# Optimization experiments

Measured on AMD Instinct MI355X. Metric: run time of the kernel, lower is better.

## Reference

```python
import jax, jax.numpy as jnp
import numpy as np

EPS = 1e-5

def conv1x1(h, w, b):
    # h: [B,C,H,W], w: [O,C], b: [O]
    return jnp.einsum('bchw,oc->bohw', h, w) + b[None, :, None, None]

def setup_inputs() -> dict:
    key = jax.random.key(0)
    ks = jax.random.split(key, 10)
    B, C, H, W = 4, 256, 64, 64
    x = jax.random.normal(ks[0], (B, C, H, W), dtype=jnp.float32)
    s = 0.02
    return {
        'x': x,
        'gamma': jnp.ones((C,), jnp.float32),
        'beta': jnp.zeros((C,), jnp.float32),
        'wq': jax.random.normal(ks[1], (C, C), jnp.float32) * s,
        'bq': jnp.zeros((C,), jnp.float32),
        'wk': jax.random.normal(ks[2], (C, C), jnp.float32) * s,
        'bk': jnp.zeros((C,), jnp.float32),
        'wv': jax.random.normal(ks[3], (C, C), jnp.float32) * s,
        'bv': jnp.zeros((C,), jnp.float32),
        'wp': jax.random.normal(ks[4], (C, C), jnp.float32) * s,
        'bp': jnp.zeros((C,), jnp.float32),
    }

def reference(x, gamma, beta, wq, bq, wk, bk, wv, bv, wp, bp):
    B, C, H, W = x.shape
    N = H * W
    # BatchNorm2d (training mode: batch statistics, biased variance)
    mean = jnp.mean(x, axis=(0, 2, 3))
    var = jnp.var(x, axis=(0, 2, 3))
    h = (x - mean[None, :, None, None]) * jax.lax.rsqrt(var + EPS)[None, :, None, None]
    h = h * gamma[None, :, None, None] + beta[None, :, None, None]
    q = conv1x1(h, wq, bq).reshape(B, C, N)
    k = conv1x1(h, wk, bk).reshape(B, C, N)
    v = conv1x1(h, wv, bv).reshape(B, C, N)
    # scores[b,i,j] = q_i . k_j, softmax over j (keys)
    scores = jnp.einsum('bci,bcj->bij', q, k) * (C ** -0.5)
    attn = jax.nn.softmax(scores, axis=2)
    # out[b,c,i] = sum_j attn[b,i,j] * v[b,c,j]
    out = jnp.einsum('bij,bcj->bci', attn, v).reshape(B, C, H, W)
    out = conv1x1(out, wp, bp)
    return x + out
```

## Files before the change

kernel.cpp:

```cpp
#include <hip/hip_runtime.h>
#include <cstdint>
#include <cstddef>

#define B_ 4
#define C_ 256
#define N_ 4096

typedef __attribute__((ext_vector_type(8))) short s8v;
typedef __attribute__((ext_vector_type(4))) float f4v;

#if defined(__has_builtin)
#if __has_builtin(__builtin_amdgcn_exp2f)
#define EXP2(x) __builtin_amdgcn_exp2f(x)
#endif
#endif
#ifndef EXP2
#define EXP2(x) exp2f(x)
#endif

__device__ __forceinline__ unsigned short f2bf(float f) {
  unsigned int u = __builtin_bit_cast(unsigned int, f);
  return (unsigned short)((u + 0x7FFFu + ((u >> 16) & 1u)) >> 16);
}

__device__ __forceinline__ unsigned pk2bf_trunc(float lo, float hi) {
  return __builtin_amdgcn_perm(__builtin_bit_cast(unsigned, hi),
                               __builtin_bit_cast(unsigned, lo), 0x07060302u);
}


__global__ __launch_bounds__(256) void bn_stats(const float* __restrict__ x,
                                                float* __restrict__ mean,
                                                float* __restrict__ rstd) {
  int c = blockIdx.x, t = threadIdx.x;
  float s = 0.f, s2 = 0.f;
  for (int b = 0; b < B_; ++b) {
    const float* p = x + ((size_t)b * C_ + c) * N_;
    for (int n = t; n < N_; n += 256) { float v = p[n]; s += v; s2 += v * v; }
  }
  __shared__ float rs[256], rs2[256];
  rs[t] = s; rs2[t] = s2; __syncthreads();
  for (int off = 128; off > 0; off >>= 1) {
    if (t < off) { rs[t] += rs[t + off]; rs2[t] += rs2[t + off]; }
    __syncthreads();
  }
  if (t == 0) {
    float m = rs[0] * (1.f / 16384.f);
    float v = rs2[0] * (1.f / 16384.f) - m * m;
    mean[c] = m; rstd[c] = rsqrtf(v + 1e-5f);
  }
}

__global__ __launch_bounds__(256) void prep(
    const float* __restrict__ wq, const float* __restrict__ bq,
    const float* __restrict__ wk, const float* __restrict__ bk,
    const float* __restrict__ wv, const float* __restrict__ bv,
    const float* __restrict__ wp,
    const float* __restrict__ gamma, const float* __restrict__ beta,
    const float* __restrict__ mean, const float* __restrict__ rstd,
    unsigned short* __restrict__ wqb, unsigned short* __restrict__ wkb,
    unsigned short* __restrict__ wvb, unsigned short* __restrict__ wpb,
    float* __restrict__ beq, float* __restrict__ bek, float* __restrict__ bev) {
  const float QSC = 0.0625f * 1.4426950408889634f;
  int o = blockIdx.x, c = threadIdx.x;
  float a = gamma[c] * rstd[c];
  float d = beta[c] - mean[c] * a;
  float wqv = wq[o * C_ + c], wkv = wk[o * C_ + c], wvv = wv[o * C_ + c];
  wqb[o * C_ + c] = f2bf(wqv * a * QSC);
  wkb[o * C_ + c] = f2bf(wkv * a);
  wvb[o * C_ + c] = f2bf(wvv * a);
  wpb[o * C_ + c] = f2bf(wp[o * C_ + c]);
  __shared__ float r0[256], r1[256], r2[256];
  r0[c] = wqv * d; r1[c] = wkv * d; r2[c] = wvv * d; __syncthreads();
  for (int off = 128; off > 0; off >>= 1) {
    if (c < off) { r0[c] += r0[c + off]; r1[c] += r1[c + off]; r2[c] += r2[c + off]; }
    __syncthreads();
  }
  if (c == 0) {
    beq[o] = (bq[o] + r0[0]) * QSC;
    bek[o] = bk[o] + r1[0];
    bev[o] = bv[o] + r2[0];
  }
}

__global__ __launch_bounds__(256) void xt(const float* __restrict__ x,
                                          unsigned short* __restrict__ xbB) {
  int b = blockIdx.z, c0 = blockIdx.y * 64, n0 = blockIdx.x * 64;
  int tid = threadIdx.x;
  __shared__ unsigned short Ls[64][72];
  int cw = tid >> 6, nl = tid & 63;
#pragma unroll
  for (int rr = 0; rr < 16; ++rr) {
    int c = c0 + cw * 16 + rr;
    Ls[nl][cw * 16 + rr] = f2bf(x[((size_t)b * C_ + c) * N_ + n0 + nl]);
  }
  __syncthreads();
  int n_ = tid >> 2, cs = (tid & 3) * 16;
  s8v v0 = *(const s8v*)(&Ls[n_][cs]);
  s8v v1 = *(const s8v*)(&Ls[n_][cs + 8]);
  int n = n0 + n_;
  size_t base = (((size_t)b * 256 + (n >> 4)) * 32 + ((c0 + cs) >> 3)) * 128 + (n & 15) * 8;
  *(s8v*)(xbB + base) = v0;
  *(s8v*)(xbB + base + 128) = v1;
}

__global__ __launch_bounds__(256) void qkv(
    const unsigned short* __restrict__ xbB,
    const unsigned short* __restrict__ wqb, const unsigned short* __restrict__ wkb,
    const unsigned short* __restrict__ wvb,
    const float* __restrict__ beq, const float* __restrict__ bek,
    const float* __restrict__ bev,
    unsigned short* __restrict__ qB, unsigned short* __restrict__ kB,
    unsigned short* __restrict__ vB) {
  int b = blockIdx.z, oblk = blockIdx.y, n0 = blockIdx.x * 64;
  int tid = threadIdx.x, w = tid >> 6, l = tid & 63, quad = l >> 4, lq = l & 15;
  int orow = oblk * 64 + w * 16 + lq;

  f4v aq[4], ak[4], av[4];
#pragma unroll
  for (int nt = 0; nt < 4; ++nt) {
    aq[nt] = (f4v){0.f, 0.f, 0.f, 0.f};
    ak[nt] = (f4v){0.f, 0.f, 0.f, 0.f};
    av[nt] = (f4v){0.f, 0.f, 0.f, 0.f};
  }

#pragma unroll
  for (int kk = 0; kk < 8; ++kk) {
    s8v afq = *(const s8v*)(wqb + (size_t)orow * C_ + kk * 32 + quad * 8);
    s8v afk = *(const s8v*)(wkb + (size_t)orow * C_ + kk * 32 + quad * 8);
    s8v afv = *(const s8v*)(wvb + (size_t)orow * C_ + kk * 32 + quad * 8);
#pragma unroll
    for (int nt = 0; nt < 4; ++nt) {
      s8v bf = *(const s8v*)(xbB + (((size_t)b * 256 + ((n0 + nt * 16) >> 4)) * 32 + kk * 4 + quad) * 128 + lq * 8);
      aq[nt] = __builtin_amdgcn_mfma_f32_16x16x32_bf16(afq, bf, aq[nt], 0, 0, 0);
      ak[nt] = __builtin_amdgcn_mfma_f32_16x16x32_bf16(afk, bf, ak[nt], 0, 0, 0);
      av[nt] = __builtin_amdgcn_mfma_f32_16x16x32_bf16(afv, bf, av[nt], 0, 0, 0);
    }
  }

  __shared__ unsigned short Ls[64][72];
  int obase = oblk * 64;

  for (int pass = 0; pass < 2; ++pass) {
    const f4v* acc = (pass == 0) ? aq : ak;
    const float* BE = (pass == 0) ? beq : bek;
    unsigned short* dst = (pass == 0) ? qB : kB;
    int ob4 = obase + w * 16 + quad * 4;
    float b0 = BE[ob4], b1 = BE[ob4 + 1], b2 = BE[ob4 + 2], b3 = BE[ob4 + 3];
#pragma unroll
    for (int nt = 0; nt < 4; ++nt) {
      unsigned lo = (unsigned)f2bf(acc[nt][0] + b0) | ((unsigned)f2bf(acc[nt][1] + b1) << 16);
      unsigned hi = (unsigned)f2bf(acc[nt][2] + b2) | ((unsigned)f2bf(acc[nt][3] + b3) << 16);
      uint2 pr; pr.x = lo; pr.y = hi;
      *(uint2*)(&Ls[nt * 16 + lq][w * 16 + quad * 4]) = pr;
    }
    __syncthreads();
    {
      int n16rel = tid >> 6, g_rel = (tid >> 3) & 7, lq2 = (tid & 7) * 2;
      s8v v0 = *(const s8v*)(&Ls[n16rel * 16 + lq2][g_rel * 8]);
      s8v v1 = *(const s8v*)(&Ls[n16rel * 16 + lq2 + 1][g_rel * 8]);
      size_t base = (((size_t)b * 256 + (n0 >> 4) + n16rel) * 32 + (obase >> 3) + g_rel) * 128 + lq2 * 8;
      *(s8v*)(dst + base) = v0;
      *(s8v*)(dst + base + 8) = v1;
    }
    __syncthreads();
  }

#pragma unroll
  for (int nt = 0; nt < 4; ++nt)
#pragma unroll
    for (int r = 0; r < 4; ++r) {
      int o_ = obase + w * 16 + quad * 4 + r;
      Ls[w * 16 + quad * 4 + r][nt * 16 + lq] = f2bf(av[nt][r] + bev[o_]);
    }
  __syncthreads();
  {
    int cb_rel = tid >> 6, hq = (tid >> 3) & 7, lq2 = (tid & 7) * 2;
    s8v v0 = *(const s8v*)(&Ls[cb_rel * 16 + lq2][hq * 8]);
    s8v v1 = *(const s8v*)(&Ls[cb_rel * 16 + lq2 + 1][hq * 8]);
    size_t base = ((((size_t)b * 64 + (n0 >> 6)) * 16 + oblk * 4 + cb_rel) * 8 + hq) * 128 + lq2 * 8;
    *(s8v*)(vB + base) = v0;
    *(s8v*)(vB + base + 8) = v1;
  }
}

__global__ __launch_bounds__(1024, 4) void attn(
    const unsigned short* __restrict__ qB, const unsigned short* __restrict__ kB,
    const unsigned short* __restrict__ vB, unsigned short* __restrict__ aB) {
  int id = blockIdx.x;
  int b = (id & 7) >> 1;
  int i0 = (((id >> 3) << 1) | (id & 1)) << 6;
  int tid = threadIdx.x, w = tid >> 6, l = tid & 63, quad = l >> 4, lq = l & 15;

  __shared__ unsigned short Qs[16384];
  __shared__ unsigned short Ps[2][16384];
  __shared__ float Lw[16][4][16];

  {
    const s8v* g = (const s8v*)(qB + ((size_t)b * 256 + (i0 >> 4)) * 4096);
    s8v* sq = (s8v*)Qs;
    sq[tid] = g[tid];
    sq[tid + 1024] = g[tid + 1024];
  }

  const unsigned short* kp = kB + (((size_t)b * 256 + w) * 32 + quad) * 128 + lq * 8;
  const unsigned short* vp = vB + ((size_t)b * 1024 + w) * 1024 + quad * 128 + lq * 8;
  const unsigned short* Qp = Qs + quad * 128 + lq * 8;
  unsigned short* Pw0 = Ps[0] + (w * 2 + (quad >> 1)) * 512 + lq * 8 + (quad & 1) * 4;
  unsigned short* Pw1 = Ps[1] + (w * 2 + (quad >> 1)) * 512 + lq * 8 + (quad & 1) * 4;
  const unsigned short* Pr0 = Ps[0] + quad * 512 + lq * 8;
  const unsigned short* Pr1 = Ps[1] + quad * 512 + lq * 8;

  s8v kf[8];
#pragma unroll
  for (int kk = 0; kk < 8; ++kk) kf[kk] = *(const s8v*)(kp + kk * 512);

  __syncthreads();

  f4v O[4];
  O[0] = (f4v){0.f, 0.f, 0.f, 0.f}; O[1] = (f4v){0.f, 0.f, 0.f, 0.f};
  O[2] = (f4v){0.f, 0.f, 0.f, 0.f}; O[3] = (f4v){0.f, 0.f, 0.f, 0.f};
  float lsum[4] = {0.f, 0.f, 0.f, 0.f};

  for (int tt = 0; tt < 8; ++tt) {
#pragma unroll
    for (int half = 0; half < 2; ++half) {
      unsigned short* Pw = half ? Pw1 : Pw0;
      const unsigned short* Pr = half ? Pr1 : Pr0;
      s8v vf[8];
#pragma unroll
      for (int ks = 0; ks < 8; ++ks)
        vf[ks] = *(const s8v*)(vp + (ks >> 1) * 16384 + (ks & 1) * 512);
#pragma unroll
      for (int rp = 0; rp < 2; ++rp) {
        f4v St0 = (f4v){0.f, 0.f, 0.f, 0.f};
        f4v St1 = (f4v){0.f, 0.f, 0.f, 0.f};
#pragma unroll
        for (int kk = 0; kk < 8; ++kk) {
          s8v q0 = *(const s8v*)(Qp + (rp * 2 + 0) * 4096 + kk * 512);
          s8v q1 = *(const s8v*)(Qp + (rp * 2 + 1) * 4096 + kk * 512);
          St0 = __builtin_amdgcn_mfma_f32_16x16x32_bf16(kf[kk], q0, St0, 0, 0, 0);
          St1 = __builtin_amdgcn_mfma_f32_16x16x32_bf16(kf[kk], q1, St1, 0, 0, 0);
        }
        {
          float e0 = EXP2(St0[0]), e1 = EXP2(St0[1]), e2 = EXP2(St0[2]), e3 = EXP2(St0[3]);
          lsum[rp * 2] += (e0 + e1) + (e2 + e3);
          uint2 pr; pr.x = pk2bf_trunc(e0, e1); pr.y = pk2bf_trunc(e2, e3);
          *(uint2*)(Pw + (rp * 2) * 128) = pr;
        }
        {
          float e0 = EXP2(St1[0]), e1 = EXP2(St1[1]), e2 = EXP2(St1[2]), e3 = EXP2(St1[3]);
          lsum[rp * 2 + 1] += (e0 + e1) + (e2 + e3);
          uint2 pr; pr.x = pk2bf_trunc(e0, e1); pr.y = pk2bf_trunc(e2, e3);
          *(uint2*)(Pw + (rp * 2 + 1) * 128) = pr;
        }
      }
      __syncthreads();
      kp += 65536;
#pragma unroll
      for (int kk = 0; kk < 8; ++kk) kf[kk] = *(const s8v*)(kp + kk * 512);
#pragma unroll
      for (int ks = 0; ks < 8; ++ks) {
        s8v p0 = *(const s8v*)(Pr + ks * 2048 + 0 * 128);
        s8v p1 = *(const s8v*)(Pr + ks * 2048 + 1 * 128);
        s8v p2 = *(const s8v*)(Pr + ks * 2048 + 2 * 128);
        s8v p3 = *(const s8v*)(Pr + ks * 2048 + 3 * 128);
        O[0] = __builtin_amdgcn_mfma_f32_16x16x32_bf16(vf[ks], p0, O[0], 0, 0, 0);
        O[1] = __builtin_amdgcn_mfma_f32_16x16x32_bf16(vf[ks], p1, O[1], 0, 0, 0);
        O[2] = __builtin_amdgcn_mfma_f32_16x16x32_bf16(vf[ks], p2, O[2], 0, 0, 0);
        O[3] = __builtin_amdgcn_mfma_f32_16x16x32_bf16(vf[ks], p3, O[3], 0, 0, 0);
      }
      vp += 65536;
    }
  }

#pragma unroll
  for (int rg = 0; rg < 4; ++rg) {
    lsum[rg] += __shfl_xor(lsum[rg], 16);
    lsum[rg] += __shfl_xor(lsum[rg], 32);
  }
  if (quad == 0) {
    Lw[w][0][lq] = lsum[0]; Lw[w][1][lq] = lsum[1];
    Lw[w][2][lq] = lsum[2]; Lw[w][3][lq] = lsum[3];
  }
  __syncthreads();
  float rl[4];
#pragma unroll
  for (int rg = 0; rg < 4; ++rg) {
    float s = 0.f;
#pragma unroll
    for (int ww = 0; ww < 16; ++ww) s += Lw[ww][rg][lq];
    rl[rg] = 1.f / s;
  }

#pragma unroll
  for (int rg = 0; rg < 4; ++rg) {
    ushort4 pk;
    pk.x = f2bf(O[rg][0] * rl[rg]);
    pk.y = f2bf(O[rg][1] * rl[rg]);
    pk.z = f2bf(O[rg][2] * rl[rg]);
    pk.w = f2bf(O[rg][3] * rl[rg]);
    size_t ob = (((size_t)b * 256 + (i0 >> 4) + rg) * 32 + w * 2 + (quad >> 1)) * 128
              + lq * 8 + (quad & 1) * 4;
    *(ushort4*)(aB + ob) = pk;
  }
}

__global__ __launch_bounds__(256) void proj(
    const float* __restrict__ x, const unsigned short* __restrict__ wpb,
    const float* __restrict__ bp, const unsigned short* __restrict__ aB,
    float* __restrict__ out) {
  int b = blockIdx.z, oblk = blockIdx.y, n0 = blockIdx.x * 64;
  int tid = threadIdx.x, w = tid >> 6, l = tid & 63, quad = l >> 4, lq = l & 15;
  int orow_a = oblk * 64 + w * 16 + lq;

  f4v acc[4];
#pragma unroll
  for (int nt = 0; nt < 4; ++nt) acc[nt] = (f4v){0.f, 0.f, 0.f, 0.f};

#pragma unroll
  for (int kk = 0; kk < 8; ++kk) {
    s8v af = *(const s8v*)(wpb + (size_t)orow_a * C_ + kk * 32 + quad * 8);
#pragma unroll
    for (int nt = 0; nt < 4; ++nt) {
      s8v bf = *(const s8v*)(aB + (((size_t)b * 256 + ((n0 + nt * 16) >> 4)) * 32 + kk * 4 + quad) * 128 + lq * 8);
      acc[nt] = __builtin_amdgcn_mfma_f32_16x16x32_bf16(af, bf, acc[nt], 0, 0, 0);
    }
  }
#pragma unroll
  for (int nt = 0; nt < 4; ++nt)
#pragma unroll
    for (int r = 0; r < 4; ++r) {
      int o_ = oblk * 64 + w * 16 + quad * 4 + r;
      size_t idx = ((size_t)b * C_ + o_) * N_ + n0 + nt * 16 + lq;
      out[idx] = x[idx] + acc[nt][r] + bp[o_];
    }
}

extern "C" void kernel_launch(void* const* d_in, const int* in_sizes, int n_in,
                              void* d_out, int out_size, void* d_ws, size_t ws_size,
                              hipStream_t stream) {
  const float* x     = (const float*)d_in[0];
  const float* gamma = (const float*)d_in[1];
  const float* beta  = (const float*)d_in[2];
  const float* wq    = (const float*)d_in[3];
  const float* bq    = (const float*)d_in[4];
  const float* wk    = (const float*)d_in[5];
  const float* bk    = (const float*)d_in[6];
  const float* wv    = (const float*)d_in[7];
  const float* bv    = (const float*)d_in[8];
  const float* wp    = (const float*)d_in[9];
  const float* bp    = (const float*)d_in[10];
  float* out = (float*)d_out;

  char* ws = (char*)d_ws;
  float* mean = (float*)ws; ws += 1024;
  float* rstd = (float*)ws; ws += 1024;
  float* beq  = (float*)ws; ws += 1024;
  float* bek  = (float*)ws; ws += 1024;
  float* bev  = (float*)ws; ws += 1024;
  unsigned short* wqb = (unsigned short*)ws; ws += C_ * C_ * 2;
  unsigned short* wkb = (unsigned short*)ws; ws += C_ * C_ * 2;
  unsigned short* wvb = (unsigned short*)ws; ws += C_ * C_ * 2;
  unsigned short* wpb = (unsigned short*)ws; ws += C_ * C_ * 2;
  unsigned short* xbB = (unsigned short*)ws; ws += (size_t)B_ * N_ * C_ * 2;
  unsigned short* qB  = (unsigned short*)ws; ws += (size_t)B_ * N_ * C_ * 2;
  unsigned short* kB  = (unsigned short*)ws; ws += (size_t)B_ * N_ * C_ * 2;
  unsigned short* vB  = (unsigned short*)ws; ws += (size_t)B_ * N_ * C_ * 2;
  unsigned short* aB  = (unsigned short*)ws; ws += (size_t)B_ * N_ * C_ * 2;

  hipLaunchKernelGGL(bn_stats, dim3(C_), dim3(256), 0, stream, x, mean, rstd);
  hipLaunchKernelGGL(prep, dim3(C_), dim3(256), 0, stream,
                     wq, bq, wk, bk, wv, bv, wp, gamma, beta, mean, rstd,
                     wqb, wkb, wvb, wpb, beq, bek, bev);
  hipLaunchKernelGGL(xt, dim3(N_ / 64, 4, B_), dim3(256), 0, stream, x, xbB);
  hipLaunchKernelGGL(qkv, dim3(N_ / 64, 4, B_), dim3(256), 0, stream,
                     xbB, wqb, wkb, wvb, beq, bek, bev, qB, kB, vB);
  hipLaunchKernelGGL(attn, dim3(256), dim3(1024), 0, stream, qB, kB, vB, aB);
  hipLaunchKernelGGL(proj, dim3(N_ / 64, 4, B_), dim3(256), 0, stream,
                     x, wpb, bp, aB, out);
}
```

Measured before the change: 211.6 us.

## Warp-specialize attention into QK/softmax producers and PV consumers using 32x32 MFMA

Rewrites the attention kernel to 512 threads in which four waves compute Q·K^T scores and exponentials into a double-buffered shared P tile, while four other waves consume the previous tile for P·V. The new kernel uses 32x32x16 MFMA instead of 16x16x32 and keeps Q in registers instead of shared memory. The qkv kernel's output layouts for q, k and v are changed to match the new fragment shapes. The aim is to overlap the score/exp phase with the PV phase and to make better use of MFMA and bandwidth. In exchange it raises register pressure, since Q takes 32 s8v per lane and there are large f16v accumulators. The producer and consumer waves can also stall on each other at every barrier.

```diff
diff --git a/kernel.cpp b/kernel.cpp
--- a/kernel.cpp
+++ b/kernel.cpp
@@ -8,6 +8,7 @@
 
 typedef __attribute__((ext_vector_type(8))) short s8v;
 typedef __attribute__((ext_vector_type(4))) float f4v;
+typedef __attribute__((ext_vector_type(16))) float f16v;
 
 #if defined(__has_builtin)
 #if __has_builtin(__builtin_amdgcn_exp2f)
@@ -26,6 +27,13 @@
 __device__ __forceinline__ unsigned pk2bf_trunc(float lo, float hi) {
   return __builtin_amdgcn_perm(__builtin_bit_cast(unsigned, hi),
                                __builtin_bit_cast(unsigned, lo), 0x07060302u);
+}
+
+__device__ __forceinline__ f16v zf16() {
+  f16v z;
+#pragma unroll
+  for (int i = 0; i < 16; ++i) z[i] = 0.f;
+  return z;
 }
 
 
@@ -144,7 +152,6 @@
   for (int pass = 0; pass < 2; ++pass) {
     const f4v* acc = (pass == 0) ? aq : ak;
     const float* BE = (pass == 0) ? beq : bek;
-    unsigned short* dst = (pass == 0) ? qB : kB;
     int ob4 = obase + w * 16 + quad * 4;
     float b0 = BE[ob4], b1 = BE[ob4 + 1], b2 = BE[ob4 + 2], b3 = BE[ob4 + 3];
 #pragma unroll
@@ -156,12 +163,19 @@
     }
     __syncthreads();
     {
-      int n16rel = tid >> 6, g_rel = (tid >> 3) & 7, lq2 = (tid & 7) * 2;
-      s8v v0 = *(const s8v*)(&Ls[n16rel * 16 + lq2][g_rel * 8]);
-      s8v v1 = *(const s8v*)(&Ls[n16rel * 16 + lq2 + 1][g_rel * 8]);
-      size_t base = (((size_t)b * 256 + (n0 >> 4) + n16rel) * 32 + (obase >> 3) + g_rel) * 128 + lq2 * 8;
-      *(s8v*)(dst + base) = v0;
-      *(s8v*)(dst + base + 8) = v1;
+      unsigned short* dp = (pass == 0) ? qB : kB;
+#pragma unroll
+      for (int ii = 0; ii < 2; ++ii) {
+        int i = tid + ii * 256;
+        int g = i >> 8, cs = (i >> 6) & 3, ll = i & 63;
+        s8v vv = *(const s8v*)(&Ls[g * 32 + (ll & 31)][cs * 16 + ((ll >> 5) << 3)]);
+        size_t dst;
+        if (pass == 0)
+          dst = ((((size_t)b * 64 + (n0 >> 6)) * 2 + g) * 16 + (obase >> 4) + cs) * 512 + (size_t)ll * 8;
+        else
+          dst = (((size_t)b * 128 + (n0 >> 5) + g) * 16 + (obase >> 4) + cs) * 512 + (size_t)ll * 8;
+        *(s8v*)(dp + dst) = vv;
+      }
     }
     __syncthreads();
   }
@@ -175,134 +189,131 @@
     }
   __syncthreads();
   {
-    int cb_rel = tid >> 6, hq = (tid >> 3) & 7, lq2 = (tid & 7) * 2;
-    s8v v0 = *(const s8v*)(&Ls[cb_rel * 16 + lq2][hq * 8]);
-    s8v v1 = *(const s8v*)(&Ls[cb_rel * 16 + lq2 + 1][hq * 8]);
-    size_t base = ((((size_t)b * 64 + (n0 >> 6)) * 16 + oblk * 4 + cb_rel) * 8 + hq) * 128 + lq2 * 8;
-    *(s8v*)(vB + base) = v0;
-    *(s8v*)(vB + base + 8) = v1;
-  }
-}
-
-__global__ __launch_bounds__(1024, 4) void attn(
+#pragma unroll
+    for (int ii = 0; ii < 2; ++ii) {
+      int i = tid + ii * 256;
+      int g = i >> 8, ks = (i >> 6) & 3, ll = i & 63;
+      s8v vv = *(const s8v*)(&Ls[g * 32 + (ll & 31)][ks * 16 + ((ll >> 5) << 3)]);
+      size_t dst = (((size_t)b * 8 + (obase >> 5) + g) * 256 + (n0 >> 4) + ks) * 512 + (size_t)ll * 8;
+      *(s8v*)(vB + dst) = vv;
+    }
+  }
+}
+
+__global__ __launch_bounds__(512, 2) void attn(
     const unsigned short* __restrict__ qB, const unsigned short* __restrict__ kB,
     const unsigned short* __restrict__ vB, unsigned short* __restrict__ aB) {
   int id = blockIdx.x;
   int b = (id & 7) >> 1;
   int i0 = (((id >> 3) << 1) | (id & 1)) << 6;
-  int tid = threadIdx.x, w = tid >> 6, l = tid & 63, quad = l >> 4, lq = l & 15;
-
-  __shared__ unsigned short Qs[16384];
+  int tid = threadIdx.x, w = tid >> 6, l = tid & 63;
+  int lh = l >> 5, l31 = l & 31;
+
   __shared__ unsigned short Ps[2][16384];
-  __shared__ float Lw[16][4][16];
-
-  {
-    const s8v* g = (const s8v*)(qB + ((size_t)b * 256 + (i0 >> 4)) * 4096);
-    s8v* sq = (s8v*)Qs;
-    sq[tid] = g[tid];
-    sq[tid + 1024] = g[tid + 1024];
-  }
-
-  const unsigned short* kp = kB + (((size_t)b * 256 + w) * 32 + quad) * 128 + lq * 8;
-  const unsigned short* vp = vB + ((size_t)b * 1024 + w) * 1024 + quad * 128 + lq * 8;
-  const unsigned short* Qp = Qs + quad * 128 + lq * 8;
-  unsigned short* Pw0 = Ps[0] + (w * 2 + (quad >> 1)) * 512 + lq * 8 + (quad & 1) * 4;
-  unsigned short* Pw1 = Ps[1] + (w * 2 + (quad >> 1)) * 512 + lq * 8 + (quad & 1) * 4;
-  const unsigned short* Pr0 = Ps[0] + quad * 512 + lq * 8;
-  const unsigned short* Pr1 = Ps[1] + quad * 512 + lq * 8;
-
-  s8v kf[8];
-#pragma unroll
-  for (int kk = 0; kk < 8; ++kk) kf[kk] = *(const s8v*)(kp + kk * 512);
-
-  __syncthreads();
-
-  f4v O[4];
-  O[0] = (f4v){0.f, 0.f, 0.f, 0.f}; O[1] = (f4v){0.f, 0.f, 0.f, 0.f};
-  O[2] = (f4v){0.f, 0.f, 0.f, 0.f}; O[3] = (f4v){0.f, 0.f, 0.f, 0.f};
-  float lsum[4] = {0.f, 0.f, 0.f, 0.f};
-
-  for (int tt = 0; tt < 8; ++tt) {
-#pragma unroll
-    for (int half = 0; half < 2; ++half) {
-      unsigned short* Pw = half ? Pw1 : Pw0;
-      const unsigned short* Pr = half ? Pr1 : Pr0;
-      s8v vf[8];
-#pragma unroll
-      for (int ks = 0; ks < 8; ++ks)
-        vf[ks] = *(const s8v*)(vp + (ks >> 1) * 16384 + (ks & 1) * 512);
-#pragma unroll
-      for (int rp = 0; rp < 2; ++rp) {
-        f4v St0 = (f4v){0.f, 0.f, 0.f, 0.f};
-        f4v St1 = (f4v){0.f, 0.f, 0.f, 0.f};
-#pragma unroll
-        for (int kk = 0; kk < 8; ++kk) {
-          s8v q0 = *(const s8v*)(Qp + (rp * 2 + 0) * 4096 + kk * 512);
-          s8v q1 = *(const s8v*)(Qp + (rp * 2 + 1) * 4096 + kk * 512);
-          St0 = __builtin_amdgcn_mfma_f32_16x16x32_bf16(kf[kk], q0, St0, 0, 0, 0);
-          St1 = __builtin_amdgcn_mfma_f32_16x16x32_bf16(kf[kk], q1, St1, 0, 0, 0);
+  __shared__ float Lw[4][2][32];
+
+  if (w < 4) {
+    s8v q[2][16];
+    {
+      const unsigned short* qp = qB + (((size_t)b * 64 + (i0 >> 6)) * 32) * 512 + (size_t)l * 8;
+#pragma unroll
+      for (int rg = 0; rg < 2; ++rg)
+#pragma unroll
+        for (int cs = 0; cs < 16; ++cs)
+          q[rg][cs] = *(const s8v*)(qp + (size_t)(rg * 16 + cs) * 512);
+    }
+    const unsigned short* kp = kB + (((size_t)b * 128 + w * 2) * 16) * 512 + (size_t)l * 8;
+    float ls0 = 0.f, ls1 = 0.f;
+
+    for (int t = 0; t < 17; ++t) {
+      if (t < 16) {
+        unsigned short* Pb = Ps[t & 1];
+#pragma unroll
+        for (int kgl = 0; kgl < 2; ++kgl) {
+          f16v St0 = zf16(), St1 = zf16();
+#pragma unroll
+          for (int half = 0; half < 2; ++half) {
+            s8v kf[8];
+#pragma unroll
+            for (int c8 = 0; c8 < 8; ++c8)
+              kf[c8] = *(const s8v*)(kp + (size_t)(kgl * 16 + half * 8 + c8) * 512);
+#pragma unroll
+            for (int c8 = 0; c8 < 8; ++c8) {
+              St0 = __builtin_amdgcn_mfma_f32_32x32x16_bf16(kf[c8], q[0][half * 8 + c8], St0, 0, 0, 0);
+              St1 = __builtin_amdgcn_mfma_f32_32x32x16_bf16(kf[c8], q[1][half * 8 + c8], St1, 0, 0, 0);
+            }
+          }
+          unsigned short* Pk = Pb + (size_t)((w * 8 + kgl * 4) * 64 + l31) * 8 + lh * 4;
+#pragma unroll
+          for (int j = 0; j < 4; ++j) {
+            float a0 = EXP2(St0[4 * j + 0]), a1 = EXP2(St0[4 * j + 1]);
+            float a2 = EXP2(St0[4 * j + 2]), a3 = EXP2(St0[4 * j + 3]);
+            ls0 += (a0 + a1) + (a2 + a3);
+            uint2 p0; p0.x = pk2bf_trunc(a0, a1); p0.y = pk2bf_trunc(a2, a3);
+            *(uint2*)(Pk + j * 512) = p0;
+            float c0 = EXP2(St1[4 * j + 0]), c1 = EXP2(St1[4 * j + 1]);
+            float c2 = EXP2(St1[4 * j + 2]), c3 = EXP2(St1[4 * j + 3]);
+            ls1 += (c0 + c1) + (c2 + c3);
+            uint2 p1; p1.x = pk2bf_trunc(c0, c1); p1.y = pk2bf_trunc(c2, c3);
+            *(uint2*)(Pk + j * 512 + 256) = p1;
+          }
         }
-        {
-          float e0 = EXP2(St0[0]), e1 = EXP2(St0[1]), e2 = EXP2(St0[2]), e3 = EXP2(St0[3]);
-          lsum[rp * 2] += (e0 + e1) + (e2 + e3);
-          uint2 pr; pr.x = pk2bf_trunc(e0, e1); pr.y = pk2bf_trunc(e2, e3);
-          *(uint2*)(Pw + (rp * 2) * 128) = pr;
-        }
-        {
-          float e0 = EXP2(St1[0]), e1 = EXP2(St1[1]), e2 = EXP2(St1[2]), e3 = EXP2(St1[3]);
-          lsum[rp * 2 + 1] += (e0 + e1) + (e2 + e3);
-          uint2 pr; pr.x = pk2bf_trunc(e0, e1); pr.y = pk2bf_trunc(e2, e3);
-          *(uint2*)(Pw + (rp * 2 + 1) * 128) = pr;
-        }
+        kp += 8 * 16 * 512;
       }
       __syncthreads();
-      kp += 65536;
-#pragma unroll
-      for (int kk = 0; kk < 8; ++kk) kf[kk] = *(const s8v*)(kp + kk * 512);
-#pragma unroll
-      for (int ks = 0; ks < 8; ++ks) {
-        s8v p0 = *(const s8v*)(Pr + ks * 2048 + 0 * 128);
-        s8v p1 = *(const s8v*)(Pr + ks * 2048 + 1 * 128);
-        s8v p2 = *(const s8v*)(Pr + ks * 2048 + 2 * 128);
-        s8v p3 = *(const s8v*)(Pr + ks * 2048 + 3 * 128);
-        O[0] = __builtin_amdgcn_mfma_f32_16x16x32_bf16(vf[ks], p0, O[0], 0, 0, 0);
-        O[1] = __builtin_amdgcn_mfma_f32_16x16x32_bf16(vf[ks], p1, O[1], 0, 0, 0);
-        O[2] = __builtin_amdgcn_mfma_f32_16x16x32_bf16(vf[ks], p2, O[2], 0, 0, 0);
-        O[3] = __builtin_amdgcn_mfma_f32_16x16x32_bf16(vf[ks], p3, O[3], 0, 0, 0);
+    }
+    ls0 += __shfl_xor(ls0, 32);
+    ls1 += __shfl_xor(ls1, 32);
+    if (l < 32) { Lw[w][0][l] = ls0; Lw[w][1][l] = ls1; }
+    __syncthreads();
+  } else {
+    int cg0 = (w - 4) * 2;
+    f16v O00 = zf16(), O01 = zf16(), O10 = zf16(), O11 = zf16();
+    const unsigned short* vp = vB + (((size_t)b * 8 + cg0) * 256) * 512 + (size_t)l * 8;
+    const unsigned short* pr_base;
+
+    for (int t = 0; t < 17; ++t) {
+      if (t > 0) {
+        pr_base = Ps[(t - 1) & 1] + (size_t)lh * 512 + l31 * 8;
+#pragma unroll
+        for (int ks = 0; ks < 16; ++ks) {
+          s8v vf0 = *(const s8v*)(vp + (size_t)ks * 512);
+          s8v vf1 = *(const s8v*)(vp + (size_t)(256 * 512) + (size_t)ks * 512);
+          s8v pf0 = *(const s8v*)(pr_base + ks * 1024);
+          s8v pf1 = *(const s8v*)(pr_base + ks * 1024 + 256);
+          O00 = __builtin_amdgcn_mfma_f32_32x32x16_bf16(vf0, pf0, O00, 0, 0, 0);
+          O01 = __builtin_amdgcn_mfma_f32_32x32x16_bf16(vf0, pf1, O01, 0, 0, 0);
+          O10 = __builtin_amdgcn_mfma_f32_32x32x16_bf16(vf1, pf0, O10, 0, 0, 0);
+          O11 = __builtin_amdgcn_mfma_f32_32x32x16_bf16(vf1, pf1, O11, 0, 0, 0);
+        }
+        vp += 16 * 512;
       }
-      vp += 65536;
-    }
-  }
-
-#pragma unroll
-  for (int rg = 0; rg < 4; ++rg) {
-    lsum[rg] += __shfl_xor(lsum[rg], 16);
-    lsum[rg] += __shfl_xor(lsum[rg], 32);
-  }
-  if (quad == 0) {
-    Lw[w][0][lq] = lsum[0]; Lw[w][1][lq] = lsum[1];
-    Lw[w][2][lq] = lsum[2]; Lw[w][3][lq] = lsum[3];
-  }
-  __syncthreads();
-  float rl[4];
-#pragma unroll
-  for (int rg = 0; rg < 4; ++rg) {
-    float s = 0.f;
-#pragma unroll
-    for (int ww = 0; ww < 16; ++ww) s += Lw[ww][rg][lq];
-    rl[rg] = 1.f / s;
-  }
-
-#pragma unroll
-  for (int rg = 0; rg < 4; ++rg) {
-    ushort4 pk;
-    pk.x = f2bf(O[rg][0] * rl[rg]);
-    pk.y = f2bf(O[rg][1] * rl[rg]);
-    pk.z = f2bf(O[rg][2] * rl[rg]);
-    pk.w = f2bf(O[rg][3] * rl[rg]);
-    size_t ob = (((size_t)b * 256 + (i0 >> 4) + rg) * 32 + w * 2 + (quad >> 1)) * 128
-              + lq * 8 + (quad & 1) * 4;
-    *(ushort4*)(aB + ob) = pk;
+      __syncthreads();
+    }
+    __syncthreads();
+    float s0 = Lw[0][0][l31] + Lw[1][0][l31] + Lw[2][0][l31] + Lw[3][0][l31];
+    float s1 = Lw[0][1][l31] + Lw[1][1][l31] + Lw[2][1][l31] + Lw[3][1][l31];
+    float rl0 = 1.f / s0, rl1 = 1.f / s1;
+#pragma unroll
+    for (int cgl = 0; cgl < 2; ++cgl) {
+      int cg = cg0 + cgl;
+#pragma unroll
+      for (int j = 0; j < 4; ++j) {
+        const f16v& Or0 = cgl ? O10 : O00;
+        const f16v& Or1 = cgl ? O11 : O01;
+        ushort4 pk;
+        pk.x = f2bf(Or0[4 * j + 0] * rl0); pk.y = f2bf(Or0[4 * j + 1] * rl0);
+        pk.z = f2bf(Or0[4 * j + 2] * rl0); pk.w = f2bf(Or0[4 * j + 3] * rl0);
+        size_t ob = (((size_t)b * 256 + (i0 >> 4) + ((l >> 4) & 1)) * 32 + cg * 4 + j) * 128
+                  + (l & 15) * 8 + lh * 4;
+        *(ushort4*)(aB + ob) = pk;
+        pk.x = f2bf(Or1[4 * j + 0] * rl1); pk.y = f2bf(Or1[4 * j + 1] * rl1);
+        pk.z = f2bf(Or1[4 * j + 2] * rl1); pk.w = f2bf(Or1[4 * j + 3] * rl1);
+        size_t ob1 = (((size_t)b * 256 + (i0 >> 4) + 2 + ((l >> 4) & 1)) * 32 + cg * 4 + j) * 128
+                   + (l & 15) * 8 + lh * 4;
+        *(ushort4*)(aB + ob1) = pk;
+      }
+    }
   }
 }
 
@@ -376,7 +387,7 @@
   hipLaunchKernelGGL(xt, dim3(N_ / 64, 4, B_), dim3(256), 0, stream, x, xbB);
   hipLaunchKernelGGL(qkv, dim3(N_ / 64, 4, B_), dim3(256), 0, stream,
                      xbB, wqb, wkb, wvb, beq, bek, bev, qB, kB, vB);
-  hipLaunchKernelGGL(attn, dim3(256), dim3(1024), 0, stream, qB, kB, vB, aB);
+  hipLaunchKernelGGL(attn, dim3(256), dim3(512), 0, stream, qB, kB, vB, aB);
   hipLaunchKernelGGL(proj, dim3(N_ / 64, 4, B_), dim3(256), 0, stream,
                      x, wpb, bp, aB, out);
 }
```

Result: slower. 232.6 us (+9.9%).
